# Performance work log

Measured on AMD Instinct MI355X. Metric: run time of the kernel, lower is better.

## Reference

```python
import jax, jax.numpy as jnp
import numpy as np

D_MODEL = 1024
NHEAD = 16
D_HEAD = D_MODEL // NHEAD
DIM_FF = 4096
EPS = 1e-5

def layer_norm(x, scale, bias):
    mu = jnp.mean(x, axis=-1, keepdims=True)
    var = jnp.mean(jnp.square(x - mu), axis=-1, keepdims=True)
    return (x - mu) * jax.lax.rsqrt(var + EPS) * scale + bias

def setup_inputs() -> dict:
    key = jax.random.key(0)
    ks = jax.random.split(key, 8)
    B, T, D = 4, 2048, D_MODEL
    s = 1.0 / np.sqrt(D)
    sf = 1.0 / np.sqrt(DIM_FF)
    return {
        "x": jax.random.normal(ks[0], (B, T, D), dtype=jnp.float32),
        "ln1_scale": jnp.ones((D,), jnp.float32),
        "ln1_bias": jnp.zeros((D,), jnp.float32),
        "qkv_w": jax.random.normal(ks[1], (3 * D, D), jnp.float32) * s,  # torch Linear weight [out,in]
        "out_w": jax.random.normal(ks[2], (D, D), jnp.float32) * s,
        "ln2_scale": jnp.ones((D,), jnp.float32),
        "ln2_bias": jnp.zeros((D,), jnp.float32),
        "fc1_w": jax.random.normal(ks[3], (DIM_FF, D), jnp.float32) * s,
        "fc1_b": jnp.zeros((DIM_FF,), jnp.float32),
        "fc2_w": jax.random.normal(ks[4], (D, DIM_FF), jnp.float32) * sf,
        "fc2_b": jnp.zeros((D,), jnp.float32),
    }

def reference(x, ln1_scale, ln1_bias, qkv_w, out_w, ln2_scale, ln2_bias, fc1_w, fc1_b, fc2_w, fc2_b):
    B, T, D = x.shape
    # --- attention sublayer (pre-LN) ---
    h = layer_norm(x, ln1_scale, ln1_bias)
    qkv = jnp.einsum('btd,ed->bte', h, qkv_w)  # [B,T,3D]
    q, k, v = jnp.split(qkv, 3, axis=-1)
    def heads(t):
        return t.reshape(B, T, NHEAD, D_HEAD).transpose(0, 2, 1, 3)  # [B,H,T,dh]
    q, k, v = heads(q), heads(k), heads(v)
    scores = jnp.einsum('bhqd,bhkd->bhqk', q, k) / np.sqrt(D_HEAD)
    attn = jax.nn.softmax(scores, axis=-1)
    o = jnp.einsum('bhqk,bhkd->bhqd', attn, v)
    o = o.transpose(0, 2, 1, 3).reshape(B, T, D)
    h = jnp.einsum('btd,ed->bte', o, out_w)
    x = x + h
    # --- FFN sublayer (pre-LN) ---
    h = layer_norm(x, ln2_scale, ln2_bias)
    h = jnp.einsum('btd,fd->btf', h, fc1_w) + fc1_b
    h = jax.nn.gelu(h, approximate=False)
    h = jnp.einsum('btf,df->btd', h, fc2_w) + fc2_b
    return x + h
```

## Files before the change

### kernel.cpp

```cpp
#include <hip/hip_runtime.h>
#include <hip/hip_bf16.h>
#include <math.h>

typedef unsigned short u16;
typedef unsigned int u32;
typedef short s8v __attribute__((ext_vector_type(8)));
typedef float f4v __attribute__((ext_vector_type(4)));
typedef float f16v __attribute__((ext_vector_type(16)));
typedef u32 u4v __attribute__((ext_vector_type(4)));
typedef u32 u2v __attribute__((ext_vector_type(2)));

#define D_MODEL 1024
#define DIMFF   4096
#define SEQ     2048
#define TOKENS  8192

#define QSCALE 0.18033688011112042f

static __device__ __forceinline__ u16 f2bf(float f) {
    unsigned int u = __builtin_bit_cast(unsigned int, f);
    unsigned int lsb = (u >> 16) & 1u;
    u += 0x7fffu + lsb;
    return (u16)(u >> 16);
}

static __device__ __forceinline__ float gelu_fast(float z) {
    float z2 = z * z;
    float p  = fmaf(z2, -0.1029472255f, -2.3021867892f);
    float e  = __builtin_amdgcn_exp2f(z * p);
    return z * __builtin_amdgcn_rcpf(1.0f + e);
}

static __device__ __forceinline__ void gl2lds16(const u16* g, u16* l) {
    __builtin_amdgcn_global_load_lds(
        (__attribute__((address_space(1))) void*)(void*)g,
        (__attribute__((address_space(3))) void*)l, 16, 0, 0);
}

static __device__ __forceinline__ void bar() {
    __builtin_amdgcn_sched_barrier(0);
    asm volatile("" ::: "memory");
    __builtin_amdgcn_s_barrier();
    asm volatile("" ::: "memory");
    __builtin_amdgcn_sched_barrier(0);
}

template<int N> static __device__ __forceinline__ void vwait() {
    if constexpr (N == 4)       asm volatile("s_waitcnt vmcnt(4)" ::: "memory");
    else if constexpr (N == 9)  asm volatile("s_waitcnt vmcnt(9)" ::: "memory");
    else if constexpr (N == 12) asm volatile("s_waitcnt vmcnt(12)" ::: "memory");
    else                        asm volatile("s_waitcnt vmcnt(0)" ::: "memory");
}

#define N4_QKV  786432
#define N4_WO   262144
#define N4_FC   1048576
__global__ __launch_bounds__(256) void cvt_all_kernel(const float* __restrict__ s0,
                                                      const float* __restrict__ s1,
                                                      const float* __restrict__ s2,
                                                      const float* __restrict__ s3,
                                                      u16* __restrict__ dst) {
    int i = blockIdx.x * 256 + threadIdx.x;
    const float* src; int j;
    if (i < N4_QKV)                    { src = s0; j = i; }
    else if (i < N4_QKV + N4_WO)       { src = s1; j = i - N4_QKV; }
    else if (i < N4_QKV + N4_WO + N4_FC) { src = s2; j = i - N4_QKV - N4_WO; }
    else                               { src = s3; j = i - N4_QKV - N4_WO - N4_FC; }
    float4 v = ((const float4*)src)[j];
    ushort4 o;
    o.x = f2bf(v.x); o.y = f2bf(v.y); o.z = f2bf(v.z); o.w = f2bf(v.w);
    ((ushort4*)dst)[i] = o;
}

__global__ __launch_bounds__(256) void ln_kernel(const float* __restrict__ x,
                                                 const float* __restrict__ scale,
                                                 const float* __restrict__ bias,
                                                 u16* __restrict__ out) {
    int row = blockIdx.x;
    int t = threadIdx.x;
    const float* xr = x + (size_t)row * D_MODEL;
    float4 v = ((const float4*)xr)[t];
    float s  = v.x + v.y + v.z + v.w;
    float ss = v.x*v.x + v.y*v.y + v.z*v.z + v.w*v.w;
    #pragma unroll
    for (int off = 1; off < 64; off <<= 1) {
        s  += __shfl_xor(s, off);
        ss += __shfl_xor(ss, off);
    }
    __shared__ float red[8];
    int wave = t >> 6, lane = t & 63;
    if (lane == 0) { red[wave] = s; red[4 + wave] = ss; }
    __syncthreads();
    float S  = red[0] + red[1] + red[2] + red[3];
    float SS = red[4] + red[5] + red[6] + red[7];
    float mu  = S * (1.0f / D_MODEL);
    float var = SS * (1.0f / D_MODEL) - mu * mu;
    float r = rsqrtf(var + 1e-5f);
    float4 sc = ((const float4*)scale)[t];
    float4 bi = ((const float4*)bias)[t];
    ushort4 o;
    o.x = f2bf((v.x - mu) * r * sc.x + bi.x);
    o.y = f2bf((v.y - mu) * r * sc.y + bi.y);
    o.z = f2bf((v.z - mu) * r * sc.z + bi.z);
    o.w = f2bf((v.w - mu) * r * sc.w + bi.w);
    ((ushort4*)(out + (size_t)row * D_MODEL))[t] = o;
}

template<int MODE, int BN_, int DEPTH>
__global__ __launch_bounds__(512, 2) void gemm_kernel(
        const u16* __restrict__ A, const u16* __restrict__ W,
        const float* __restrict__ bias, const float* __restrict__ res,
        void* __restrict__ outp, void* __restrict__ out2, int M, int N, int K) {
    constexpr int BM = 256, BK = 32;
    constexpr int NFN = BN_ / 64;
    constexpr int RA = 2;
    constexpr int RB = BN_ / 128;
    constexpr int S = DEPTH - 1;
    constexpr int VST = (S - 2) * (RA + RB);
    constexpr int ASZ = BM * BK, BSZ = BN_ * BK;
    __shared__ __attribute__((aligned(16))) u16 As[DEPTH * ASZ];
    __shared__ __attribute__((aligned(16))) u16 Bs[DEPTH * BSZ];

    int t = threadIdx.x;
    int lane = t & 63, w = t >> 6;
    int lc = lane & 15, lr = lane >> 4;
    int nb = N / BN_;
    int cpx = gridDim.x >> 3;
    int blk = (blockIdx.x & 7) * cpx + (blockIdx.x >> 3);
    int bm = blk / nb, bn = blk % nb;
    int m0 = bm * BM, n0 = bn * BN_;
    int wm = (w >> 2) * 128;
    int wn = (w & 3) * (BN_ / 4);
    int cxor = (lr ^ ((lc >> 1) & 3)) * 8;

    const u16* Abase = A + (size_t)m0 * K;
    const u16* Bbase = W + (size_t)n0 * K;

    size_t aoff[RA]; int aldo[RA];
    #pragma unroll
    for (int n = 0; n < RA; ++n) {
        int q = (n * 8 + w) * 64 + lane;
        int row = q >> 2;
        aoff[n] = (size_t)row * K + (((q & 3) ^ ((row >> 1) & 3)) * 8);
        aldo[n] = (n * 8 + w) * 512;
    }
    size_t boff[RB]; int bldo[RB];
    #pragma unroll
    for (int n = 0; n < RB; ++n) {
        int q = (n * 8 + w) * 64 + lane;
        int row = q >> 2;
        boff[n] = (size_t)row * K + (((q & 3) ^ ((row >> 1) & 3)) * 8);
        bldo[n] = (n * 8 + w) * 512;
    }

    const int NT = K / BK;
    for (int u = 0; u < S; ++u) {
        size_t kk = (size_t)u * BK;
        #pragma unroll
        for (int n = 0; n < RA; ++n) gl2lds16(Abase + aoff[n] + kk, &As[u * ASZ + aldo[n]]);
        #pragma unroll
        for (int n = 0; n < RB; ++n) gl2lds16(Bbase + boff[n] + kk, &Bs[u * BSZ + bldo[n]]);
    }
    vwait<VST>();
    bar();

    f4v acc[8][NFN] = {};
    s8v afA[8], bA_[NFN], afB[8], bB_[NFN];
    #pragma unroll
    for (int i = 0; i < 8; ++i)
        afA[i] = *(const s8v*)&As[(wm + i * 16 + lc) * BK + cxor];
    #pragma unroll
    for (int j = 0; j < NFN; ++j)
        bA_[j] = *(const s8v*)&Bs[(wn + j * 16 + lc) * BK + cxor];
    int rs = 1, ss = S;

#define GSTEP(T, AFL, BL, AFC, BC)                                            \
    {                                                                         \
        const u16* Ab = &As[rs * ASZ];                                        \
        const u16* Bb = &Bs[rs * BSZ];                                        \
        _Pragma("unroll")                                                     \
        for (int i = 0; i < 8; ++i)                                           \
            AFL[i] = *(const s8v*)&Ab[(wm + i * 16 + lc) * BK + cxor];        \
        _Pragma("unroll")                                                     \
        for (int j = 0; j < NFN; ++j)                                         \
            BL[j] = *(const s8v*)&Bb[(wn + j * 16 + lc) * BK + cxor];         \
        int kts = (T) + S; if (kts > NT - 1) kts = NT - 1;                    \
        size_t kk = (size_t)kts * BK;                                         \
        _Pragma("unroll")                                                     \
        for (int n = 0; n < RA; ++n)                                          \
            gl2lds16(Abase + aoff[n] + kk, &As[ss * ASZ + aldo[n]]);          \
        _Pragma("unroll")                                                     \
        for (int n = 0; n < RB; ++n)                                          \
            gl2lds16(Bbase + boff[n] + kk, &Bs[ss * BSZ + bldo[n]]);          \
        __builtin_amdgcn_s_setprio(1);                                        \
        _Pragma("unroll")                                                     \
        for (int i = 0; i < 8; ++i) {                                         \
            _Pragma("unroll")                                                 \
            for (int j = 0; j < NFN; ++j) {                                   \
                if constexpr (MODE == 4)                                      \
                    acc[i][j] = __builtin_amdgcn_mfma_f32_16x16x32_bf16(AFC[i], BC[j], acc[i][j], 0, 0, 0); \
                else                                                          \
                    acc[i][j] = __builtin_amdgcn_mfma_f32_16x16x32_bf16(BC[j], AFC[i], acc[i][j], 0, 0, 0); \
            }                                                                 \
        }                                                                     \
        __builtin_amdgcn_s_setprio(0);                                        \
        vwait<VST>();                                                         \
        bar();                                                                \
        rs = (rs + 1 == DEPTH) ? 0 : rs + 1;                                  \
        ss = (ss + 1 == DEPTH) ? 0 : ss + 1;                                  \
    }

    for (int kt = 0; kt < NT; kt += 2) {
        GSTEP(kt,     afB, bB_, afA, bA_)
        GSTEP(kt + 1, afA, bA_, afB, bB_)
    }
#undef GSTEP

    if constexpr (MODE == 4) {
        #pragma unroll
        for (int i = 0; i < 8; ++i) {
            #pragma unroll
            for (int j = 0; j < NFN; ++j) {
                int col = n0 + wn + j * 16 + lc;
                int colbase = n0 + wn + j * 16;
                if (colbase < 2048) {
                    float sc = (colbase < 1024) ? QSCALE : 1.0f;
                    #pragma unroll
                    for (int r = 0; r < 4; ++r) {
                        int row = m0 + wm + i * 16 + lr * 4 + r;
                        ((u16*)outp)[(size_t)row * 2048 + col] = f2bf(acc[i][j][r] * sc);
                    }
                } else {
                    int dlin = col - 2048;
                    int h = dlin >> 6, dd = dlin & 63;
                    int trow = m0 + wm + i * 16 + lr * 4;
                    int bb = trow >> 11, tt = trow & 2047;
                    int bh = bb * 16 + h;
                    ushort4 vv;
                    vv.x = f2bf(acc[i][j][0]); vv.y = f2bf(acc[i][j][1]);
                    vv.z = f2bf(acc[i][j][2]); vv.w = f2bf(acc[i][j][3]);
                    *(ushort4*)&((u16*)out2)[((size_t)bh * 64 + dd) * SEQ + tt] = vv;
                }
            }
        }
    } else {
        #pragma unroll
        for (int j = 0; j < NFN; ++j) {
            int colb = n0 + wn + j * 16 + lr * 4;
            float4 b4;
            if constexpr (MODE != 1) b4 = *(const float4*)&bias[colb];
            #pragma unroll
            for (int i = 0; i < 8; ++i) {
                int row = m0 + wm + i * 16 + lc;
                size_t idx = (size_t)row * N + colb;
                f4v a = acc[i][j];
                if constexpr (MODE == 2) {
                    ushort4 o;
                    o.x = f2bf(gelu_fast(a[0] + b4.x));
                    o.y = f2bf(gelu_fast(a[1] + b4.y));
                    o.z = f2bf(gelu_fast(a[2] + b4.z));
                    o.w = f2bf(gelu_fast(a[3] + b4.w));
                    *(ushort4*)&((u16*)outp)[idx] = o;
                } else {
                    float4 rr = *(const float4*)&res[idx];
                    float4 o;
                    if constexpr (MODE == 3) {
                        o.x = rr.x + a[0] + b4.x; o.y = rr.y + a[1] + b4.y;
                        o.z = rr.z + a[2] + b4.z; o.w = rr.w + a[3] + b4.w;
                    } else {
                        o.x = rr.x + a[0]; o.y = rr.y + a[1];
                        o.z = rr.z + a[2]; o.w = rr.w + a[3];
                    }
                    *(float4*)&((float*)outp)[idx] = o;
                }
            }
        }
    }
}

__global__ __launch_bounds__(256) void attn_kernel(const u16* __restrict__ qk,
                                                   const u16* __restrict__ vt,
                                                   u16* __restrict__ out) {
    __shared__ __attribute__((aligned(16))) u16 Ks[64 * 64];
    __shared__ __attribute__((aligned(16))) u16 Vts[64 * 64];
    __shared__ float l_s[128];
    int t = threadIdx.x, lane = t & 63, w = t >> 6;
    int l31 = lane & 31, hi = lane >> 5;
    int blk = blockIdx.x;
    int bh = blk & 63, qt = blk >> 6;
    int b = bh >> 4, h = bh & 15;
    size_t tok0 = (size_t)b * SEQ;
    int q0 = qt * 128;

    s8v bq[4];
    {
        const u16* qp = qk + (tok0 + q0 + w * 32 + l31) * 2048 + h * 64 + hi * 8;
        #pragma unroll
        for (int dch = 0; dch < 4; ++dch) bq[dch] = *(const s8v*)(qp + dch * 16);
    }
    f16v o[2] = {};
    float lp = 0.f;

    int srow[2], scg[2];
    #pragma unroll
    for (int n = 0; n < 2; ++n) {
        int chunk = (w * 2 + n) * 64 + lane;
        srow[n] = chunk >> 3;
        scg[n]  = ((chunk & 7) ^ (srow[n] & 7)) * 8;
    }
    const u16* vbase = vt + (size_t)bh * 64 * SEQ;

    for (int kt = 0; kt < SEQ / 64; ++kt) {
        #pragma unroll
        for (int n = 0; n < 2; ++n) {
            gl2lds16(&qk[(tok0 + kt * 64 + srow[n]) * 2048 + 1024 + h * 64 + scg[n]],
                     &Ks[(w * 2 + n) * 512]);
            gl2lds16(&vbase[(size_t)srow[n] * SEQ + kt * 64 + scg[n]],
                     &Vts[(w * 2 + n) * 512]);
        }
        __syncthreads();

        f16v s_[2] = {};
        #pragma unroll
        for (int kb = 0; kb < 2; ++kb)
            #pragma unroll
            for (int dch = 0; dch < 4; ++dch) {
                s8v ak = *(const s8v*)&Ks[(kb * 32 + l31) * 64 + ((dch * 2 + hi) ^ (l31 & 7)) * 8];
                s_[kb] = __builtin_amdgcn_mfma_f32_32x32x16_bf16(ak, bq[dch], s_[kb], 0, 0, 0);
            }

        u2v pk[2][4];
        #pragma unroll
        for (int kb = 0; kb < 2; ++kb)
            #pragma unroll
            for (int g = 0; g < 4; ++g) {
                u32 ib[4];
                #pragma unroll
                for (int rr = 0; rr < 4; ++rr) {
                    ib[rr] = (u32)fmaf(s_[kb][g * 4 + rr], 8388608.0f, 1064992506.0f);
                    lp += __builtin_bit_cast(float, ib[rr]);
                }
                pk[kb][g][0] = __builtin_amdgcn_perm(ib[1], ib[0], 0x07060302);
                pk[kb][g][1] = __builtin_amdgcn_perm(ib[3], ib[2], 0x07060302);
            }

        #pragma unroll
        for (int ch = 0; ch < 4; ++ch) {
            int kb = ch >> 1, a2 = (ch & 1) * 2;
            u2v sx = __builtin_amdgcn_permlane32_swap(pk[kb][a2][0], pk[kb][a2 + 1][0], false, false);
            u2v sy = __builtin_amdgcn_permlane32_swap(pk[kb][a2][1], pk[kb][a2 + 1][1], false, false);
            u4v tmp; tmp.x = sx[0]; tmp.y = sy[0]; tmp.z = sx[1]; tmp.w = sy[1];
            s8v ap = __builtin_bit_cast(s8v, tmp);
            #pragma unroll
            for (int dblk = 0; dblk < 2; ++dblk) {
                s8v bv = *(const s8v*)&Vts[(dblk * 32 + l31) * 64 + ((ch * 2 + hi) ^ (l31 & 7)) * 8];
                o[dblk] = __builtin_amdgcn_mfma_f32_32x32x16_bf16(ap, bv, o[dblk], 0, 0, 0);
            }
        }
        __syncthreads();
    }

    lp += __shfl_xor(lp, 32);
    l_s[w * 32 + l31] = 1.0f / lp;
    #pragma unroll
    for (int r = 0; r < 16; ++r) {
        int qrl = (r & 3) + 8 * (r >> 2) + 4 * hi;
        float linv = l_s[w * 32 + qrl];
        size_t row = tok0 + q0 + w * 32 + qrl;
        #pragma unroll
        for (int dblk = 0; dblk < 2; ++dblk)
            out[row * 1024 + h * 64 + dblk * 32 + l31] = f2bf(o[dblk][r] * linv);
    }
}

extern "C" void kernel_launch(void* const* d_in, const int* in_sizes, int n_in,
                              void* d_out, int out_size, void* d_ws, size_t ws_size,
                              hipStream_t stream) {
    const float* x      = (const float*)d_in[0];
    const float* ln1_s  = (const float*)d_in[1];
    const float* ln1_b  = (const float*)d_in[2];
    const float* qkv_w  = (const float*)d_in[3];
    const float* out_w  = (const float*)d_in[4];
    const float* ln2_s  = (const float*)d_in[5];
    const float* ln2_b  = (const float*)d_in[6];
    const float* fc1_w  = (const float*)d_in[7];
    const float* fc1_b  = (const float*)d_in[8];
    const float* fc2_w  = (const float*)d_in[9];
    const float* fc2_b  = (const float*)d_in[10];
    float* out = (float*)d_out;

    char* ws = (char*)d_ws;
    size_t off = 0;
    auto alloc = [&](size_t bytes) -> void* {
        void* p = ws + off;
        off += (bytes + 255) & ~(size_t)255;
        return p;
    };
    u16* wq  = (u16*)alloc((size_t)3072 * 1024 * 2);
    u16* wo  = (u16*)alloc((size_t)1024 * 1024 * 2);
    u16* w1  = (u16*)alloc((size_t)4096 * 1024 * 2);
    u16* w2  = (u16*)alloc((size_t)1024 * 4096 * 2);
    u16* h1  = (u16*)alloc((size_t)TOKENS * 1024 * 2);
    u16* qk  = (u16*)alloc((size_t)TOKENS * 2048 * 2);
    float* x2 = (float*)alloc((size_t)TOKENS * 1024 * 4);
    u16* g   = (u16*)alloc((size_t)TOKENS * 4096 * 2);
    u16* attn_out = h1;
    u16* h2       = qk;
    u16* vt       = (u16*)x2;
    (void)wo; (void)w1; (void)w2;

    cvt_all_kernel<<<(N4_QKV + N4_WO + 2 * N4_FC) / 256, 256, 0, stream>>>(
        qkv_w, out_w, fc1_w, fc2_w, wq);

    ln_kernel<<<TOKENS, 256, 0, stream>>>(x, ln1_s, ln1_b, h1);
    gemm_kernel<4, 256, 4><<<(TOKENS / 256) * (3072 / 256), 512, 0, stream>>>(
        h1, wq, nullptr, nullptr, qk, vt, TOKENS, 3072, 1024);
    attn_kernel<<<64 * 16, 256, 0, stream>>>(qk, vt, attn_out);
    gemm_kernel<1, 128, 6><<<(TOKENS / 256) * (1024 / 128), 512, 0, stream>>>(
        attn_out, wo, nullptr, x, x2, nullptr, TOKENS, 1024, 1024);
    ln_kernel<<<TOKENS, 256, 0, stream>>>(x2, ln2_s, ln2_b, h2);
    gemm_kernel<2, 256, 4><<<(TOKENS / 256) * (DIMFF / 256), 512, 0, stream>>>(
        h2, w1, fc1_b, nullptr, g, nullptr, TOKENS, DIMFF, 1024);
    gemm_kernel<3, 128, 6><<<(TOKENS / 256) * (1024 / 128), 512, 0, stream>>>(
        g, w2, fc2_b, x2, out, nullptr, TOKENS, 1024, DIMFF);
}
```

Measured before the change: 483.5 us.

## Unify GEMMs on 256x128 tiles with 4x2 wave layout and XCD-aware block mapping

Drops the BN template parameter so every GEMM uses a fixed 256x128 block tile with six pipeline stages. Waves are rearranged from a 2x4 grid of 128xBN/4 subtiles into a 4x2 grid of 64x64 subtiles, and block indices are remapped so each XCD owns a contiguous group of four M-tiles, iterating N within it. The QKV and FC1 GEMMs move from 256-wide to 128-wide N tiles, giving more blocks and a deeper pipeline at the cost of lower arithmetic intensity per block. The new mapping hardcodes four M-tiles per XCD, which matches TOKENS/256 = 32 M-tiles spread over 8 XCDs.

```diff
diff --git a/kernel.cpp b/kernel.cpp
--- a/kernel.cpp
+++ b/kernel.cpp
@@ -106,15 +106,14 @@
     ((ushort4*)(out + (size_t)row * D_MODEL))[t] = o;
 }
 
-template<int MODE, int BN_, int DEPTH>
+template<int MODE, int DEPTH>
 __global__ __launch_bounds__(512, 2) void gemm_kernel(
         const u16* __restrict__ A, const u16* __restrict__ W,
         const float* __restrict__ bias, const float* __restrict__ res,
         void* __restrict__ outp, void* __restrict__ out2, int M, int N, int K) {
-    constexpr int BM = 256, BK = 32;
-    constexpr int NFN = BN_ / 64;
+    constexpr int BM = 256, BN_ = 128, BK = 32;
     constexpr int RA = 2;
-    constexpr int RB = BN_ / 128;
+    constexpr int RB = 1;
     constexpr int S = DEPTH - 1;
     constexpr int VST = (S - 2) * (RA + RB);
     constexpr int ASZ = BM * BK, BSZ = BN_ * BK;
@@ -125,12 +124,12 @@
     int lane = t & 63, w = t >> 6;
     int lc = lane & 15, lr = lane >> 4;
     int nb = N / BN_;
-    int cpx = gridDim.x >> 3;
-    int blk = (blockIdx.x & 7) * cpx + (blockIdx.x >> 3);
-    int bm = blk / nb, bn = blk % nb;
+    int xcd = blockIdx.x & 7, li = blockIdx.x >> 3;
+    int bm = xcd * 4 + (li & 3), bn = li >> 2;
+    (void)nb;
     int m0 = bm * BM, n0 = bn * BN_;
-    int wm = (w >> 2) * 128;
-    int wn = (w & 3) * (BN_ / 4);
+    int wm = (w & 3) * 64;
+    int wn = (w >> 2) * 64;
     int cxor = (lr ^ ((lc >> 1) & 3)) * 8;
 
     const u16* Abase = A + (size_t)m0 * K;
@@ -144,13 +143,12 @@
         aoff[n] = (size_t)row * K + (((q & 3) ^ ((row >> 1) & 3)) * 8);
         aldo[n] = (n * 8 + w) * 512;
     }
-    size_t boff[RB]; int bldo[RB];
-    #pragma unroll
-    for (int n = 0; n < RB; ++n) {
-        int q = (n * 8 + w) * 64 + lane;
+    size_t boff; int bldo;
+    {
+        int q = w * 64 + lane;
         int row = q >> 2;
-        boff[n] = (size_t)row * K + (((q & 3) ^ ((row >> 1) & 3)) * 8);
-        bldo[n] = (n * 8 + w) * 512;
+        boff = (size_t)row * K + (((q & 3) ^ ((row >> 1) & 3)) * 8);
+        bldo = w * 512;
     }
 
     const int NT = K / BK;
@@ -158,19 +156,18 @@
         size_t kk = (size_t)u * BK;
         #pragma unroll
         for (int n = 0; n < RA; ++n) gl2lds16(Abase + aoff[n] + kk, &As[u * ASZ + aldo[n]]);
-        #pragma unroll
-        for (int n = 0; n < RB; ++n) gl2lds16(Bbase + boff[n] + kk, &Bs[u * BSZ + bldo[n]]);
+        gl2lds16(Bbase + boff + kk, &Bs[u * BSZ + bldo]);
     }
     vwait<VST>();
     bar();
 
-    f4v acc[8][NFN] = {};
-    s8v afA[8], bA_[NFN], afB[8], bB_[NFN];
-    #pragma unroll
-    for (int i = 0; i < 8; ++i)
+    f4v acc[4][4] = {};
+    s8v afA[4], bA_[4], afB[4], bB_[4];
+    #pragma unroll
+    for (int i = 0; i < 4; ++i)
         afA[i] = *(const s8v*)&As[(wm + i * 16 + lc) * BK + cxor];
     #pragma unroll
-    for (int j = 0; j < NFN; ++j)
+    for (int j = 0; j < 4; ++j)
         bA_[j] = *(const s8v*)&Bs[(wn + j * 16 + lc) * BK + cxor];
     int rs = 1, ss = S;
 
@@ -179,24 +176,22 @@
         const u16* Ab = &As[rs * ASZ];                                        \
         const u16* Bb = &Bs[rs * BSZ];                                        \
         _Pragma("unroll")                                                     \
-        for (int i = 0; i < 8; ++i)                                           \
+        for (int i = 0; i < 4; ++i)                                           \
             AFL[i] = *(const s8v*)&Ab[(wm + i * 16 + lc) * BK + cxor];        \
         _Pragma("unroll")                                                     \
-        for (int j = 0; j < NFN; ++j)                                         \
+        for (int j = 0; j < 4; ++j)                                           \
             BL[j] = *(const s8v*)&Bb[(wn + j * 16 + lc) * BK + cxor];         \
         int kts = (T) + S; if (kts > NT - 1) kts = NT - 1;                    \
         size_t kk = (size_t)kts * BK;                                         \
         _Pragma("unroll")                                                     \
         for (int n = 0; n < RA; ++n)                                          \
             gl2lds16(Abase + aoff[n] + kk, &As[ss * ASZ + aldo[n]]);          \
-        _Pragma("unroll")                                                     \
-        for (int n = 0; n < RB; ++n)                                          \
-            gl2lds16(Bbase + boff[n] + kk, &Bs[ss * BSZ + bldo[n]]);          \
+        gl2lds16(Bbase + boff + kk, &Bs[ss * BSZ + bldo]);                    \
         __builtin_amdgcn_s_setprio(1);                                        \
         _Pragma("unroll")                                                     \
-        for (int i = 0; i < 8; ++i) {                                         \
+        for (int i = 0; i < 4; ++i) {                                         \
             _Pragma("unroll")                                                 \
-            for (int j = 0; j < NFN; ++j) {                                   \
+            for (int j = 0; j < 4; ++j) {                                     \
                 if constexpr (MODE == 4)                                      \
                     acc[i][j] = __builtin_amdgcn_mfma_f32_16x16x32_bf16(AFC[i], BC[j], acc[i][j], 0, 0, 0); \
                 else                                                          \
@@ -218,9 +213,9 @@
 
     if constexpr (MODE == 4) {
         #pragma unroll
-        for (int i = 0; i < 8; ++i) {
+        for (int i = 0; i < 4; ++i) {
             #pragma unroll
-            for (int j = 0; j < NFN; ++j) {
+            for (int j = 0; j < 4; ++j) {
                 int col = n0 + wn + j * 16 + lc;
                 int colbase = n0 + wn + j * 16;
                 if (colbase < 2048) {
@@ -245,12 +240,12 @@
         }
     } else {
         #pragma unroll
-        for (int j = 0; j < NFN; ++j) {
+        for (int j = 0; j < 4; ++j) {
             int colb = n0 + wn + j * 16 + lr * 4;
             float4 b4;
             if constexpr (MODE != 1) b4 = *(const float4*)&bias[colb];
             #pragma unroll
-            for (int i = 0; i < 8; ++i) {
+            for (int i = 0; i < 4; ++i) {
                 int row = m0 + wm + i * 16 + lc;
                 size_t idx = (size_t)row * N + colb;
                 f4v a = acc[i][j];
@@ -413,14 +408,14 @@
         qkv_w, out_w, fc1_w, fc2_w, wq);
 
     ln_kernel<<<TOKENS, 256, 0, stream>>>(x, ln1_s, ln1_b, h1);
-    gemm_kernel<4, 256, 4><<<(TOKENS / 256) * (3072 / 256), 512, 0, stream>>>(
+    gemm_kernel<4, 6><<<(TOKENS / 256) * (3072 / 128), 512, 0, stream>>>(
         h1, wq, nullptr, nullptr, qk, vt, TOKENS, 3072, 1024);
     attn_kernel<<<64 * 16, 256, 0, stream>>>(qk, vt, attn_out);
-    gemm_kernel<1, 128, 6><<<(TOKENS / 256) * (1024 / 128), 512, 0, stream>>>(
+    gemm_kernel<1, 6><<<(TOKENS / 256) * (1024 / 128), 512, 0, stream>>>(
         attn_out, wo, nullptr, x, x2, nullptr, TOKENS, 1024, 1024);
     ln_kernel<<<TOKENS, 256, 0, stream>>>(x2, ln2_s, ln2_b, h2);
-    gemm_kernel<2, 256, 4><<<(TOKENS / 256) * (DIMFF / 256), 512, 0, stream>>>(
+    gemm_kernel<2, 6><<<(TOKENS / 256) * (DIMFF / 128), 512, 0, stream>>>(
         h2, w1, fc1_b, nullptr, g, nullptr, TOKENS, DIMFF, 1024);
-    gemm_kernel<3, 128, 6><<<(TOKENS / 256) * (1024 / 128), 512, 0, stream>>>(
+    gemm_kernel<3, 6><<<(TOKENS / 256) * (1024 / 128), 512, 0, stream>>>(
         g, w2, fc2_b, x2, out, nullptr, TOKENS, 1024, DIMFF);
 }
```

After: 482.2 us. No clear change (-0.3%).
